# Optimization experiments

Measured on AMD Instinct MI355X. Metric: run time of the kernel, lower is better.

## Reference

```python
import jax, jax.numpy as jnp
import numpy as np

N_NODES = 10000
N_EDGES = 640000
IN_CH = 128
HID = 256
OUT_CH = 10
NUM_GRAPHS = 64
EPS = 0.0  # non-trainable buffer, initial_eps=0


def setup_inputs() -> dict:
    key = jax.random.key(0)
    ks = jax.random.split(key, 12)
    x = jax.random.normal(ks[0], (N_NODES, IN_CH), dtype=jnp.float32)
    edge_index = jax.random.randint(ks[1], (2, N_EDGES), 0, N_NODES, dtype=jnp.int64)
    batch = jnp.sort(jax.random.randint(ks[2], (N_NODES,), 0, NUM_GRAPHS, dtype=jnp.int64))
    edge_weights = jax.random.uniform(ks[3], (N_EDGES,), dtype=jnp.float32)
    def lin(k, fan_in, fan_out):
        bound = 1.0 / np.sqrt(fan_in)
        kw, kb = jax.random.split(k)
        W = jax.random.uniform(kw, (fan_out, fan_in), minval=-bound, maxval=bound, dtype=jnp.float32)
        b = jax.random.uniform(kb, (fan_out,), minval=-bound, maxval=bound, dtype=jnp.float32)
        return W, b
    W1, b1 = lin(ks[4], IN_CH, HID)
    W2, b2 = lin(ks[5], HID, HID)
    W3, b3 = lin(ks[6], HID, HID)
    Wl, bl = lin(ks[7], HID, OUT_CH)
    return {"x": x, "edge_index": edge_index, "batch": batch, "edge_weights": edge_weights,
            "W1": W1, "b1": b1, "W2": W2, "b2": b2, "W3": W3, "b3": b3, "Wl": Wl, "bl": bl}


def _ginw_conv(x, edge_index, edge_weights, W, b):
    # message: edge_weight * x_j (source nodes), aggregated by add at target i
    src, dst = edge_index[0], edge_index[1]
    msg = edge_weights[:, None] * x[src]           # [E, F]
    agg = jax.ops.segment_sum(msg, dst, num_segments=N_NODES)  # [N, F]
    out = agg + (1.0 + EPS) * x
    return out @ W.T + b


def reference(x, edge_index, batch, edge_weights, W1, b1, W2, b2, W3, b3, Wl, bl):
    h = jax.nn.relu(_ginw_conv(x, edge_index, edge_weights, W1, b1))
    h = jax.nn.relu(_ginw_conv(h, edge_index, edge_weights, W2, b2))
    h = jax.nn.relu(_ginw_conv(h, edge_index, edge_weights, W3, b3))
    # global mean pool over graphs
    sums = jax.ops.segment_sum(h, batch, num_segments=NUM_GRAPHS)        # [G, HID]
    cnts = jax.ops.segment_sum(jnp.ones((N_NODES,), h.dtype), batch, num_segments=NUM_GRAPHS)
    pooled = sums / jnp.maximum(cnts, 1.0)[:, None]
    return pooled @ Wl.T + bl
```

## Files before the change

kernel.cpp:

```cpp
#include <hip/hip_runtime.h>
#include <hip/hip_fp16.h>

namespace {
constexpr int NN   = 10000;
constexpr int NE   = 640000;
constexpr int INC  = 128;
constexpr int HIDC = 256;
constexpr int OUTC = 10;
constexpr int NG   = 64;
constexpr int PP   = 8;

constexpr int NB     = 157;
constexpr int G1     = 256;
constexpr int CHUNK1 = NE / G1;
constexpr int CAPB   = 64;
constexpr int LCAP   = 5120;
}

typedef __attribute__((ext_vector_type(8))) short short8;
typedef __attribute__((ext_vector_type(4))) float f32x4;

__device__ __forceinline__ ushort f2bf(float f) {
    uint u = __float_as_uint(f);
    uint r = u + 0x7FFFu + ((u >> 16) & 1u);
    return (ushort)(r >> 16);
}
__device__ __forceinline__ float bf2f(ushort u) {
    return __uint_as_float(((uint)u) << 16);
}
__device__ __forceinline__ float rec_w(uint rec) {
    return __half2float(__ushort_as_half((ushort)(rec & 0xFFFFu)));
}

__global__ __launch_bounds__(256) void partition_kernel(const int* __restrict__ ei,
                                                        const float* __restrict__ ew,
                                                        uint2* __restrict__ stag,
                                                        int* __restrict__ cnts,
                                                        int* __restrict__ cnts_T,
                                                        const float* __restrict__ x,
                                                        ushort* __restrict__ xb) {
    __shared__ int lcnt[NB];
    const int t = threadIdx.x, g = blockIdx.x;
    for (int i = t; i < NB; i += 256) lcnt[i] = 0;
    __syncthreads();
    const int base = g * CHUNK1;
    for (int i = t; i < CHUNK1; i += 256) {
        const int e = base + i;
        const int dst = ei[NE + e];
        const int src = ei[e];
        const ushort hw = __half_as_ushort(__float2half(ew[e]));
        const int bk = dst >> 6;
        const int idx = atomicAdd(&lcnt[bk], 1);
        if (idx < CAPB)
            stag[((size_t)g * NB + bk) * CAPB + idx] =
                make_uint2(((uint)src << 16) | (uint)hw, (uint)dst);
    }
    __syncthreads();
    for (int i = t; i < NB; i += 256) {
        const int c = min(lcnt[i], CAPB);
        cnts[g * NB + i] = c;
        cnts_T[i * G1 + g] = c;
    }
    const int total4 = NN * INC / 4;
    for (int i = g * 256 + t; i < total4; i += G1 * 256) {
        float4 v = ((const float4*)x)[i];
        ushort4 o;
        o.x = f2bf(v.x); o.y = f2bf(v.y); o.z = f2bf(v.z); o.w = f2bf(v.w);
        ((ushort4*)xb)[i] = o;
    }
}

__global__ __launch_bounds__(256) void bucketscan_kernel(const int* __restrict__ cnts_T,
                                                         int* __restrict__ bucket_start,
                                                         int* __restrict__ row_start) {
    __shared__ int part[256];
    const int t = threadIdx.x;
    int s = 0;
    if (t < NB) {
        const int4* r = (const int4*)(cnts_T + (size_t)t * G1);
#pragma unroll 8
        for (int i = 0; i < G1 / 4; i++) {
            int4 v = r[i];
            s += v.x + v.y + v.z + v.w;
        }
    }
    part[t] = s;
    __syncthreads();
    for (int off = 1; off < 256; off <<= 1) {
        int v = (t >= off) ? part[t - off] : 0;
        __syncthreads();
        part[t] += v;
        __syncthreads();
    }
    if (t < NB) bucket_start[t] = part[t] - s;
    if (t == 0) {
        bucket_start[NB] = part[255];
        row_start[NN] = part[255];
    }
}

__global__ __launch_bounds__(256) void place_kernel(const uint2* __restrict__ stag,
                                                    const int* __restrict__ cnts,
                                                    const int* __restrict__ bucket_start,
                                                    int* __restrict__ row_start,
                                                    uint* __restrict__ erec) {
    const int b = blockIdx.x;
    const int t = threadIdx.x;
    __shared__ int part[256];
    __shared__ int foff[G1 + 1];
    __shared__ int h[64];
    __shared__ int curl[64];
    __shared__ uint2 srec[LCAP];

    const int c = cnts[t * NB + b];
    part[t] = c;
    if (t < 64) h[t] = 0;
    __syncthreads();
    for (int off = 1; off < 256; off <<= 1) {
        int v = (t >= off) ? part[t - off] : 0;
        __syncthreads();
        part[t] += v;
        __syncthreads();
    }
    foff[t] = part[t] - c;
    if (t == 255) foff[G1] = part[255];
    __syncthreads();
    const int Rb = foff[G1];

    for (int r = t; r < Rb; r += 256) {
        int lo = 0, hi = G1;
        while (hi - lo > 1) { int mid = (lo + hi) >> 1; if (foff[mid] <= r) lo = mid; else hi = mid; }
        uint2 rec = stag[((size_t)lo * NB + b) * CAPB + (r - foff[lo])];
        if (r < LCAP) srec[r] = rec;
        atomicAdd(&h[rec.y & 63], 1);
    }
    __syncthreads();

    const int hv = (t < 64) ? h[t] : 0;
    part[t] = hv;
    __syncthreads();
    for (int off = 1; off < 256; off <<= 1) {
        int v = (t >= off) ? part[t - off] : 0;
        __syncthreads();
        part[t] += v;
        __syncthreads();
    }
    const int bs = bucket_start[b];
    if (t < 64) {
        const int excl = part[t] - hv;
        const int node = b * 64 + t;
        if (node < NN) row_start[node] = bs + excl;
        curl[t] = excl;
    }
    __syncthreads();

    for (int r = t; r < Rb; r += 256) {
        uint2 rec;
        if (r < LCAP) rec = srec[r];
        else {
            int lo = 0, hi = G1;
            while (hi - lo > 1) { int mid = (lo + hi) >> 1; if (foff[mid] <= r) lo = mid; else hi = mid; }
            rec = stag[((size_t)lo * NB + b) * CAPB + (r - foff[lo])];
        }
        const int pos = bs + atomicAdd(&curl[rec.y & 63], 1);
        erec[pos] = rec.x;
    }
}

template <int F>
__global__ __launch_bounds__(256) void gather_bf16_kernel(const int* __restrict__ row_start,
                                                          const uint* __restrict__ erec,
                                                          const ushort* __restrict__ x,
                                                          ushort* __restrict__ out) {
    constexpr int VEC = F / 64;
    constexpr int U = 12;
    const int n = blockIdx.x * 4 + (threadIdx.x >> 6);
    const int lane = threadIdx.x & 63;
    if (n >= NN) return;
    const int beg = row_start[n];
    const int end = row_start[n + 1];
    const size_t loff = (size_t)lane * VEC;

    float acc[VEC];
    {
        ushort v[VEC];
        if (VEC == 4) *(ushort4*)v = *(const ushort4*)(x + (size_t)n * F + loff);
        else          *(ushort2*)v = *(const ushort2*)(x + (size_t)n * F + loff);
#pragma unroll
        for (int i = 0; i < VEC; i++) acc[i] = bf2f(v[i]);
    }

    int e = beg;
    for (; e + U <= end; e += U) {
        uint rec[U];
#pragma unroll
        for (int u = 0; u < U; u++) rec[u] = erec[e + u];
        ushort v[U][VEC];
#pragma unroll
        for (int u = 0; u < U; u++) {
            const ushort* r = x + (size_t)(rec[u] >> 16) * F + loff;
            if (VEC == 4) *(ushort4*)v[u] = *(const ushort4*)r;
            else          *(ushort2*)v[u] = *(const ushort2*)r;
        }
#pragma unroll
        for (int u = 0; u < U; u++) {
            const float w = rec_w(rec[u]);
#pragma unroll
            for (int i = 0; i < VEC; i++) acc[i] += w * bf2f(v[u][i]);
        }
    }
    for (; e < end; e++) {
        uint rec = erec[e];
        const float w = rec_w(rec);
        ushort v[VEC];
        const ushort* r = x + (size_t)(rec >> 16) * F + loff;
        if (VEC == 4) *(ushort4*)v = *(const ushort4*)r;
        else          *(ushort2*)v = *(const ushort2*)r;
#pragma unroll
        for (int i = 0; i < VEC; i++) acc[i] += w * bf2f(v[i]);
    }

    ushort o[VEC];
#pragma unroll
    for (int i = 0; i < VEC; i++) o[i] = f2bf(acc[i]);
    if (VEC == 4) *(ushort4*)(out + (size_t)n * F + loff) = *(ushort4*)o;
    else          *(ushort2*)(out + (size_t)n * F + loff) = *(ushort2*)o;
}

template <int K>
__global__ __launch_bounds__(256) void mfma_gemm_kernel(const ushort* __restrict__ A,
                                                        const float* __restrict__ W,
                                                        const float* __restrict__ bias,
                                                        ushort* __restrict__ C, int M) {
    constexpr int LDW = K + 8;
    __shared__ ushort Ws[64 * LDW];
    const int tid = threadIdx.x;
    const int bm = blockIdx.x * 128;
    const int bn = blockIdx.y * 64;

    constexpr int CPR = K / 4;
    for (int idx = tid; idx < 64 * CPR; idx += 256) {
        int r = idx / CPR, c = idx % CPR;
        float4 v = *(const float4*)(W + (size_t)(bn + r) * K + c * 4);
        ushort4 o;
        o.x = f2bf(v.x); o.y = f2bf(v.y); o.z = f2bf(v.z); o.w = f2bf(v.w);
        *(ushort4*)(&Ws[r * LDW + c * 4]) = o;
    }
    __syncthreads();

    const int wave = tid >> 6;
    const int lane = tid & 63;
    const int lrow = lane & 15;
    const int lq   = lane >> 4;
    const int m0 = bm + wave * 32;

    f32x4 acc[2][4] = {};
    const int r0 = min(m0 + lrow, M - 1);
    const int r1 = min(m0 + 16 + lrow, M - 1);

    for (int k0 = 0; k0 < K; k0 += 32) {
        const int kk = k0 + lq * 8;
        short8 a0 = *(const short8*)(A + (size_t)r0 * K + kk);
        short8 a1 = *(const short8*)(A + (size_t)r1 * K + kk);
        short8 b[4];
#pragma unroll
        for (int j = 0; j < 4; j++)
            b[j] = *(const short8*)(&Ws[(j * 16 + lrow) * LDW + kk]);
#pragma unroll
        for (int j = 0; j < 4; j++) {
            acc[0][j] = __builtin_amdgcn_mfma_f32_16x16x32_bf16(a0, b[j], acc[0][j], 0, 0, 0);
            acc[1][j] = __builtin_amdgcn_mfma_f32_16x16x32_bf16(a1, b[j], acc[1][j], 0, 0, 0);
        }
    }

#pragma unroll
    for (int sub = 0; sub < 2; sub++) {
#pragma unroll
        for (int j = 0; j < 4; j++) {
            const int gn = bn + j * 16 + lrow;
            const float bv = bias[gn];
#pragma unroll
            for (int i = 0; i < 4; i++) {
                const int gm = m0 + sub * 16 + lq * 4 + i;
                if (gm < M) {
                    float v = acc[sub][j][i] + bv;
                    v = fmaxf(v, 0.0f);
                    C[(size_t)gm * HIDC + gn] = f2bf(v);
                }
            }
        }
    }
}

__device__ __forceinline__ int lower_bound_batch(const int* __restrict__ batch, int val) {
    int lo = 0, hi = NN;
    while (lo < hi) {
        int mid = (lo + hi) >> 1;
        if (batch[mid] < val) lo = mid + 1;
        else hi = mid;
    }
    return lo;
}

__global__ __launch_bounds__(256) void pool_partial_kernel(const ushort* __restrict__ h,
                                                           const int* __restrict__ batch,
                                                           float* __restrict__ partials) {
    const int g = blockIdx.x;
    const int p = blockIdx.y;
    const int c = threadIdx.x;
    const int lo = lower_bound_batch(batch, g);
    const int hi = lower_bound_batch(batch, g + 1);
    const int cnt = hi - lo;
    const int chunk = (cnt + PP - 1) / PP;
    const int n0 = lo + p * chunk;
    const int n1 = min(hi, n0 + chunk);
    float sum = 0.0f;
    for (int n = n0; n < n1; n++) sum += bf2f(h[(size_t)n * HIDC + c]);
    partials[((size_t)g * PP + p) * HIDC + c] = sum;
}

__global__ __launch_bounds__(256) void head_kernel(const float* __restrict__ partials,
                                                   const int* __restrict__ batch,
                                                   const float* __restrict__ Wl,
                                                   const float* __restrict__ bl,
                                                   float* __restrict__ out) {
    __shared__ float s[HIDC];
    const int g = blockIdx.x;
    const int c = threadIdx.x;
    const int lo = lower_bound_batch(batch, g);
    const int hi = lower_bound_batch(batch, g + 1);
    const float inv = 1.0f / fmaxf((float)(hi - lo), 1.0f);
    float sum = 0.0f;
#pragma unroll
    for (int p = 0; p < PP; p++) sum += partials[((size_t)g * PP + p) * HIDC + c];
    s[c] = sum * inv;
    __syncthreads();
    if (c < OUTC) {
        float acc = bl[c];
        for (int k = 0; k < HIDC; k++) acc += s[k] * Wl[(size_t)c * HIDC + k];
        out[(size_t)g * OUTC + c] = acc;
    }
}

extern "C" void kernel_launch(void* const* d_in, const int* in_sizes, int n_in,
                              void* d_out, int out_size, void* d_ws, size_t ws_size,
                              hipStream_t stream) {
    const float* x     = (const float*)d_in[0];
    const int*   ei    = (const int*)d_in[1];
    const int*   batch = (const int*)d_in[2];
    const float* ew    = (const float*)d_in[3];
    const float* W1    = (const float*)d_in[4];
    const float* b1    = (const float*)d_in[5];
    const float* W2    = (const float*)d_in[6];
    const float* b2    = (const float*)d_in[7];
    const float* W3    = (const float*)d_in[8];
    const float* b3    = (const float*)d_in[9];
    const float* Wl    = (const float*)d_in[10];
    const float* bl    = (const float*)d_in[11];

    char* p = (char*)d_ws;
    uint2*  stag   = (uint2*)p;  p += (size_t)G1 * NB * CAPB * 8;
    ushort* xb     = (ushort*)p; p += (size_t)NN * INC * 2;
    ushort* agg128 = (ushort*)p; p += (size_t)NN * INC * 2;
    ushort* agg256 = (ushort*)p; p += (size_t)NN * HIDC * 2;
    ushort* h      = (ushort*)p; p += (size_t)NN * HIDC * 2;
    uint*   erec   = (uint*)p;   p += (size_t)NE * 4;
    float*  partials = (float*)p; p += (size_t)NG * PP * HIDC * 4;
    int*    cnts   = (int*)p;    p += (size_t)G1 * NB * 4;
    int*    cnts_T = (int*)p;    p += (size_t)NB * G1 * 4;
    int*    bucket_start = (int*)p; p += 1024;
    int*    row_start = (int*)p; p += 40016;

    partition_kernel<<<G1, 256, 0, stream>>>(ei, ew, stag, cnts, cnts_T, x, xb);
    bucketscan_kernel<<<1, 256, 0, stream>>>(cnts_T, bucket_start, row_start);
    place_kernel<<<NB, 256, 0, stream>>>(stag, cnts, bucket_start, row_start, erec);

    const int gather_grid = (NN + 3) / 4;
    dim3 gemm_grid((NN + 127) / 128, HIDC / 64);

    gather_bf16_kernel<INC><<<gather_grid, 256, 0, stream>>>(row_start, erec, xb, agg128);
    mfma_gemm_kernel<INC><<<gemm_grid, 256, 0, stream>>>(agg128, W1, b1, h, NN);

    gather_bf16_kernel<HIDC><<<gather_grid, 256, 0, stream>>>(row_start, erec, h, agg256);
    mfma_gemm_kernel<HIDC><<<gemm_grid, 256, 0, stream>>>(agg256, W2, b2, h, NN);

    gather_bf16_kernel<HIDC><<<gather_grid, 256, 0, stream>>>(row_start, erec, h, agg256);
    mfma_gemm_kernel<HIDC><<<gemm_grid, 256, 0, stream>>>(agg256, W3, b3, h, NN);

    pool_partial_kernel<<<dim3(NG, PP), 256, 0, stream>>>(h, batch, partials);
    head_kernel<<<NG, 256, 0, stream>>>(partials, batch, Wl, bl, (float*)d_out);
}
```

Before: 261.4 us.

## Fold bucket scan into place kernel and split 256-wide gathers by feature half

Removes the separate single-block bucketscan launch. Each place_kernel block now recomputes the global bucket prefix scan from cnts_T itself, and the block size goes up to 1024 threads for record placement. The 256-channel gathers switch to a new kernel that splits the feature dimension into two 128-wide halves over a second grid dimension, with a 16-edge unrolled load batch per lane. This trades one launch and a serial dependency for redundant scan work in every block, and doubles the edge-record reads in exchange for more parallel blocks and more loads in flight.

```diff
diff --git a/kernel.cpp b/kernel.cpp
--- a/kernel.cpp
+++ b/kernel.cpp
@@ -70,40 +70,11 @@
     }
 }
 
-__global__ __launch_bounds__(256) void bucketscan_kernel(const int* __restrict__ cnts_T,
-                                                         int* __restrict__ bucket_start,
-                                                         int* __restrict__ row_start) {
-    __shared__ int part[256];
-    const int t = threadIdx.x;
-    int s = 0;
-    if (t < NB) {
-        const int4* r = (const int4*)(cnts_T + (size_t)t * G1);
-#pragma unroll 8
-        for (int i = 0; i < G1 / 4; i++) {
-            int4 v = r[i];
-            s += v.x + v.y + v.z + v.w;
-        }
-    }
-    part[t] = s;
-    __syncthreads();
-    for (int off = 1; off < 256; off <<= 1) {
-        int v = (t >= off) ? part[t - off] : 0;
-        __syncthreads();
-        part[t] += v;
-        __syncthreads();
-    }
-    if (t < NB) bucket_start[t] = part[t] - s;
-    if (t == 0) {
-        bucket_start[NB] = part[255];
-        row_start[NN] = part[255];
-    }
-}
-
-__global__ __launch_bounds__(256) void place_kernel(const uint2* __restrict__ stag,
-                                                    const int* __restrict__ cnts,
-                                                    const int* __restrict__ bucket_start,
-                                                    int* __restrict__ row_start,
-                                                    uint* __restrict__ erec) {
+__global__ __launch_bounds__(1024) void place_kernel(const uint2* __restrict__ stag,
+                                                     const int* __restrict__ cnts,
+                                                     const int* __restrict__ cnts_T,
+                                                     int* __restrict__ row_start,
+                                                     uint* __restrict__ erec) {
     const int b = blockIdx.x;
     const int t = threadIdx.x;
     __shared__ int part[256];
@@ -112,22 +83,50 @@
     __shared__ int curl[64];
     __shared__ uint2 srec[LCAP];
 
-    const int c = cnts[t * NB + b];
-    part[t] = c;
-    if (t < 64) h[t] = 0;
-    __syncthreads();
-    for (int off = 1; off < 256; off <<= 1) {
-        int v = (t >= off) ? part[t - off] : 0;
+    {
+        int s = 0;
+        if (t < NB) {
+            const int4* r = (const int4*)(cnts_T + (size_t)t * G1);
+#pragma unroll 8
+            for (int i = 0; i < G1 / 4; i++) {
+                int4 v = r[i];
+                s += v.x + v.y + v.z + v.w;
+            }
+        }
+        if (t < 256) part[t] = s;
         __syncthreads();
-        part[t] += v;
+        for (int off = 1; off < 256; off <<= 1) {
+            int v = 0;
+            if (t < 256 && t >= off) v = part[t - off];
+            __syncthreads();
+            if (t < 256) part[t] += v;
+            __syncthreads();
+        }
+    }
+    const int bs = (b == 0) ? 0 : part[b - 1];
+    if (b == 0 && t == 0) row_start[NN] = part[NB - 1];
+    __syncthreads();
+
+    {
+        int c = 0;
+        if (t < 256) c = cnts[t * NB + b];
+        if (t < 256) part[t] = c;
+        if (t < 64) h[t] = 0;
         __syncthreads();
-    }
-    foff[t] = part[t] - c;
-    if (t == 255) foff[G1] = part[255];
-    __syncthreads();
+        for (int off = 1; off < 256; off <<= 1) {
+            int v = 0;
+            if (t < 256 && t >= off) v = part[t - off];
+            __syncthreads();
+            if (t < 256) part[t] += v;
+            __syncthreads();
+        }
+        if (t < 256) foff[t] = part[t] - c;
+        if (t == 0) foff[G1] = part[255];
+        __syncthreads();
+    }
     const int Rb = foff[G1];
 
-    for (int r = t; r < Rb; r += 256) {
+    for (int r = t; r < Rb; r += 1024) {
         int lo = 0, hi = G1;
         while (hi - lo > 1) { int mid = (lo + hi) >> 1; if (foff[mid] <= r) lo = mid; else hi = mid; }
         uint2 rec = stag[((size_t)lo * NB + b) * CAPB + (r - foff[lo])];
@@ -136,25 +135,27 @@
     }
     __syncthreads();
 
-    const int hv = (t < 64) ? h[t] : 0;
-    part[t] = hv;
-    __syncthreads();
-    for (int off = 1; off < 256; off <<= 1) {
-        int v = (t >= off) ? part[t - off] : 0;
+    {
+        const int hv = (t < 64) ? h[t] : 0;
+        if (t < 256) part[t] = (t < 64) ? hv : 0;
         __syncthreads();
-        part[t] += v;
+        for (int off = 1; off < 64; off <<= 1) {
+            int v = 0;
+            if (t < 256 && t >= off) v = part[t - off];
+            __syncthreads();
+            if (t < 256) part[t] += v;
+            __syncthreads();
+        }
+        if (t < 64) {
+            const int excl = part[t] - hv;
+            const int node = b * 64 + t;
+            if (node < NN) row_start[node] = bs + excl;
+            curl[t] = excl;
+        }
         __syncthreads();
     }
-    const int bs = bucket_start[b];
-    if (t < 64) {
-        const int excl = part[t] - hv;
-        const int node = b * 64 + t;
-        if (node < NN) row_start[node] = bs + excl;
-        curl[t] = excl;
-    }
-    __syncthreads();
-
-    for (int r = t; r < Rb; r += 256) {
+
+    for (int r = t; r < Rb; r += 1024) {
         uint2 rec;
         if (r < LCAP) rec = srec[r];
         else {
@@ -225,6 +226,55 @@
     for (int i = 0; i < VEC; i++) o[i] = f2bf(acc[i]);
     if (VEC == 4) *(ushort4*)(out + (size_t)n * F + loff) = *(ushort4*)o;
     else          *(ushort2*)(out + (size_t)n * F + loff) = *(ushort2*)o;
+}
+
+__global__ __launch_bounds__(256) void gather_bf16_half_kernel(const int* __restrict__ row_start,
+                                                               const uint* __restrict__ erec,
+                                                               const ushort* __restrict__ x,
+                                                               ushort* __restrict__ out) {
+    constexpr int U = 16;
+    const int n = blockIdx.x * 4 + (threadIdx.x >> 6);
+    const int lane = threadIdx.x & 63;
+    if (n >= NN) return;
+    const int beg = row_start[n];
+    const int end = row_start[n + 1];
+    const size_t loff = (size_t)blockIdx.y * 128 + lane * 2;
+
+    float acc[2];
+    {
+        ushort2 v = *(const ushort2*)(x + (size_t)n * HIDC + loff);
+        acc[0] = bf2f(v.x);
+        acc[1] = bf2f(v.y);
+    }
+
+    int e = beg;
+    for (; e + U <= end; e += U) {
+        uint rec[U];
+#pragma unroll
+        for (int u = 0; u < U; u++) rec[u] = erec[e + u];
+        ushort2 v[U];
+#pragma unroll
+        for (int u = 0; u < U; u++)
+            v[u] = *(const ushort2*)(x + (size_t)(rec[u] >> 16) * HIDC + loff);
+#pragma unroll
+        for (int u = 0; u < U; u++) {
+            const float w = rec_w(rec[u]);
+            acc[0] += w * bf2f(v[u].x);
+            acc[1] += w * bf2f(v[u].y);
+        }
+    }
+    for (; e < end; e++) {
+        uint rec = erec[e];
+        const float w = rec_w(rec);
+        ushort2 v = *(const ushort2*)(x + (size_t)(rec >> 16) * HIDC + loff);
+        acc[0] += w * bf2f(v.x);
+        acc[1] += w * bf2f(v.y);
+    }
+
+    ushort2 o;
+    o.x = f2bf(acc[0]);
+    o.y = f2bf(acc[1]);
+    *(ushort2*)(out + (size_t)n * HIDC + loff) = o;
 }
 
 template <int K>
@@ -368,12 +418,10 @@
     float*  partials = (float*)p; p += (size_t)NG * PP * HIDC * 4;
     int*    cnts   = (int*)p;    p += (size_t)G1 * NB * 4;
     int*    cnts_T = (int*)p;    p += (size_t)NB * G1 * 4;
-    int*    bucket_start = (int*)p; p += 1024;
     int*    row_start = (int*)p; p += 40016;
 
     partition_kernel<<<G1, 256, 0, stream>>>(ei, ew, stag, cnts, cnts_T, x, xb);
-    bucketscan_kernel<<<1, 256, 0, stream>>>(cnts_T, bucket_start, row_start);
-    place_kernel<<<NB, 256, 0, stream>>>(stag, cnts, bucket_start, row_start, erec);
+    place_kernel<<<NB, 1024, 0, stream>>>(stag, cnts, cnts_T, row_start, erec);
 
     const int gather_grid = (NN + 3) / 4;
     dim3 gemm_grid((NN + 127) / 128, HIDC / 64);
@@ -381,10 +429,10 @@
     gather_bf16_kernel<INC><<<gather_grid, 256, 0, stream>>>(row_start, erec, xb, agg128);
     mfma_gemm_kernel<INC><<<gemm_grid, 256, 0, stream>>>(agg128, W1, b1, h, NN);
 
-    gather_bf16_kernel<HIDC><<<gather_grid, 256, 0, stream>>>(row_start, erec, h, agg256);
+    gather_bf16_half_kernel<<<dim3(gather_grid, 2), 256, 0, stream>>>(row_start, erec, h, agg256);
     mfma_gemm_kernel<HIDC><<<gemm_grid, 256, 0, stream>>>(agg256, W2, b2, h, NN);
 
-    gather_bf16_kernel<HIDC><<<gather_grid, 256, 0, stream>>>(row_start, erec, h, agg256);
+    gather_bf16_half_kernel<<<dim3(gather_grid, 2), 256, 0, stream>>>(row_start, erec, h, agg256);
     mfma_gemm_kernel<HIDC><<<gemm_grid, 256, 0, stream>>>(agg256, W3, b3, h, NN);
 
     pool_partial_kernel<<<dim3(NG, PP), 256, 0, stream>>>(h, batch, partials);
```

After: 242.3 us. 1.08x faster.
